# Performance work log

Hardware: AMD Instinct MI355X
Metric: run time of the kernel (lower is better)

Reference implementation:

```python
import jax, jax.numpy as jnp
import numpy as np

B, T, D = 8, 4096, 1024
TRUNC = 8


def setup_inputs() -> dict:
    key = jax.random.key(0)
    k1, k2, k3, k4 = jax.random.split(key, 4)
    inputs = jax.random.normal(k1, (B, T, D), dtype=jnp.float32)
    rou = jax.random.uniform(k2, (D,), dtype=jnp.float32)
    a = jax.random.uniform(k3, (D,), dtype=jnp.float32) * 0.8
    b = jax.random.uniform(k4, (D,), dtype=jnp.float32) * 0.3
    return {"inputs": inputs, "rou": rou, "a": a, "b": b, "truncation_steps": TRUNC}


def reference(inputs, rou, a, b, truncation_steps):
    # inputs: [B, T, D] -> seq: [B, D, T]; time is the last axis
    seq = jnp.swapaxes(inputs, 1, 2)
    r_ = rou[None, :, None]
    a_ = a[None, :, None]
    b_ = b[None, :, None]
    prefix = r_ * (1.0 - b_ * seq)          # [B, D, T]
    drive = (1.0 - r_) * a_ * seq           # [B, D, T]
    T_ = seq.shape[-1]
    # truncated LIF scan: out[t] = sum_{k=0..K} drive[t-k] * prod_{o=1..k} prefix[t-k+o]
    out = drive
    running = drive
    for k in range(1, truncation_steps + 1):
        running = running[..., : T_ - k] * prefix[..., k:]  # length T-k
        out = out.at[..., k:].add(running)
    return jnp.swapaxes(out, 1, 2)          # [B, T, D]
```

## Files before the change

kernel.cpp:

```cpp
#include <hip/hip_runtime.h>


#define B_ 8
#define T_ 4096
#define D_ 1024
#define TRUNC_ 8
#define TC 64
#define NCHUNK (T_ / TC)
#define D4 (D_ / 4)

__global__ __launch_bounds__(256) void lif_kernel(
    const float* __restrict__ x,
    const float* __restrict__ rou,
    const float* __restrict__ a,
    const float* __restrict__ bparm,
    float* __restrict__ out)
{
    const int tid   = threadIdx.x;
    const int chunk = blockIdx.x % NCHUNK;
    const int batch = blockIdx.x / NCHUNK;
    const int t0    = chunk * TC;
    const int tw    = (t0 >= TRUNC_) ? (t0 - TRUNC_) : 0;
    const int tend  = t0 + TC;

    const float4 rv = reinterpret_cast<const float4*>(rou)[tid];
    const float4 av = reinterpret_cast<const float4*>(a)[tid];
    const float4 bv = reinterpret_cast<const float4*>(bparm)[tid];

    float rr[4] = {rv.x, rv.y, rv.z, rv.w};
    float bc[4] = {bv.x, bv.y, bv.z, bv.w};
    float cc[4] = {(1.0f - rv.x) * av.x,
                   (1.0f - rv.y) * av.y,
                   (1.0f - rv.z) * av.z,
                   (1.0f - rv.w) * av.w};

    float r[4][9];
#pragma unroll
    for (int ch = 0; ch < 4; ++ch)
#pragma unroll
        for (int k = 0; k < 9; ++k) r[ch][k] = 0.0f;

    const float4* __restrict__ xin =
        reinterpret_cast<const float4*>(x) + (size_t)batch * T_ * D4;
    float4* __restrict__ op =
        reinterpret_cast<float4*>(out) + (size_t)batch * T_ * D4;

    auto step = [&](const float4 xv) -> float4 {
        float xs[4] = {xv.x, xv.y, xv.z, xv.w};
        float os[4];
#pragma unroll
        for (int ch = 0; ch < 4; ++ch) {
            const float p  = rr[ch] * (1.0f - bc[ch] * xs[ch]);
            const float dr = cc[ch] * xs[ch];
#pragma unroll
            for (int k = 8; k >= 1; --k) r[ch][k] = r[ch][k - 1] * p;
            r[ch][0] = dr;
            float s = dr;
#pragma unroll
            for (int k = 1; k <= 8; ++k) s += r[ch][k];
            os[ch] = s;
        }
        return make_float4(os[0], os[1], os[2], os[3]);
    };

    for (int t = tw; t < t0; ++t) {
        (void)step(xin[(size_t)t * D4 + tid]);
    }

    for (int t = t0; t < tend; t += 4) {
        const size_t i0 = (size_t)t * D4 + tid;
        float4 x0 = xin[i0];
        float4 x1 = xin[i0 + D4];
        float4 x2 = xin[i0 + 2 * D4];
        float4 x3 = xin[i0 + 3 * D4];
        float4 o0 = step(x0);
        float4 o1 = step(x1);
        float4 o2 = step(x2);
        float4 o3 = step(x3);
        op[i0]          = o0;
        op[i0 + D4]     = o1;
        op[i0 + 2 * D4] = o2;
        op[i0 + 3 * D4] = o3;
    }
}

extern "C" void kernel_launch(void* const* d_in, const int* in_sizes, int n_in,
                              void* d_out, int out_size, void* d_ws, size_t ws_size,
                              hipStream_t stream) {
    const float* x    = (const float*)d_in[0];
    const float* rou  = (const float*)d_in[1];
    const float* a    = (const float*)d_in[2];
    const float* bprm = (const float*)d_in[3];
    float* out        = (float*)d_out;

    dim3 grid(B_ * NCHUNK);
    dim3 block(256);
    lif_kernel<<<grid, block, 0, stream>>>(x, rou, a, bprm, out);
}
```

Measured before the change: 48.00 us.

## Double time chunk, batch eight loads ahead of compute, use nontemporal stores

```diff
diff --git a/kernel.cpp b/kernel.cpp
--- a/kernel.cpp
+++ b/kernel.cpp
@@ -5,9 +5,11 @@
 #define T_ 4096
 #define D_ 1024
 #define TRUNC_ 8
-#define TC 64
+#define TC 128
 #define NCHUNK (T_ / TC)
 #define D4 (D_ / 4)
+
+typedef float vf4 __attribute__((ext_vector_type(4)));
 
 __global__ __launch_bounds__(256) void lif_kernel(
     const float* __restrict__ x,
@@ -23,9 +25,9 @@
     const int tw    = (t0 >= TRUNC_) ? (t0 - TRUNC_) : 0;
     const int tend  = t0 + TC;
 
-    const float4 rv = reinterpret_cast<const float4*>(rou)[tid];
-    const float4 av = reinterpret_cast<const float4*>(a)[tid];
-    const float4 bv = reinterpret_cast<const float4*>(bparm)[tid];
+    const vf4 rv = reinterpret_cast<const vf4*>(rou)[tid];
+    const vf4 av = reinterpret_cast<const vf4*>(a)[tid];
+    const vf4 bv = reinterpret_cast<const vf4*>(bparm)[tid];
 
     float rr[4] = {rv.x, rv.y, rv.z, rv.w};
     float bc[4] = {bv.x, bv.y, bv.z, bv.w};
@@ -40,12 +42,12 @@
 #pragma unroll
         for (int k = 0; k < 9; ++k) r[ch][k] = 0.0f;
 
-    const float4* __restrict__ xin =
-        reinterpret_cast<const float4*>(x) + (size_t)batch * T_ * D4;
-    float4* __restrict__ op =
-        reinterpret_cast<float4*>(out) + (size_t)batch * T_ * D4;
+    const vf4* __restrict__ xin =
+        reinterpret_cast<const vf4*>(x) + (size_t)batch * T_ * D4;
+    vf4* __restrict__ op =
+        reinterpret_cast<vf4*>(out) + (size_t)batch * T_ * D4;
 
-    auto step = [&](const float4 xv) -> float4 {
+    auto step = [&](const vf4 xv) -> vf4 {
         float xs[4] = {xv.x, xv.y, xv.z, xv.w};
         float os[4];
 #pragma unroll
@@ -60,27 +62,26 @@
             for (int k = 1; k <= 8; ++k) s += r[ch][k];
             os[ch] = s;
         }
-        return make_float4(os[0], os[1], os[2], os[3]);
+        vf4 o; o.x = os[0]; o.y = os[1]; o.z = os[2]; o.w = os[3];
+        return o;
     };
 
     for (int t = tw; t < t0; ++t) {
         (void)step(xin[(size_t)t * D4 + tid]);
     }
 
-    for (int t = t0; t < tend; t += 4) {
+    for (int t = t0; t < tend; t += 8) {
         const size_t i0 = (size_t)t * D4 + tid;
-        float4 x0 = xin[i0];
-        float4 x1 = xin[i0 + D4];
-        float4 x2 = xin[i0 + 2 * D4];
-        float4 x3 = xin[i0 + 3 * D4];
-        float4 o0 = step(x0);
-        float4 o1 = step(x1);
-        float4 o2 = step(x2);
-        float4 o3 = step(x3);
-        op[i0]          = o0;
-        op[i0 + D4]     = o1;
-        op[i0 + 2 * D4] = o2;
-        op[i0 + 3 * D4] = o3;
+        vf4 xv[8];
+#pragma unroll
+        for (int u = 0; u < 8; ++u) xv[u] = xin[i0 + (size_t)u * D4];
+        __builtin_amdgcn_sched_barrier(0);
+        vf4 ov[8];
+#pragma unroll
+        for (int u = 0; u < 8; ++u) ov[u] = step(xv[u]);
+#pragma unroll
+        for (int u = 0; u < 8; ++u)
+            __builtin_nontemporal_store(ov[u], &op[i0 + (size_t)u * D4]);
     }
 }
 
```

After: 46.33 us. -3.5%, faster.
